# Kernel optimization log

Hardware: AMD Instinct MI355X
Metric: run time of the kernel (lower is better)

## Reference

```python
import jax, jax.numpy as jnp
import numpy as np

WS = (2, 7, 7)      # window size
SS = (1, 3, 3)      # shift size
NH = 8              # num heads
DIM = 256
N = WS[0] * WS[1] * WS[2]   # 98 tokens per window
EPS = 1e-5


def _ln(x, w, b):
    m = jnp.mean(x, -1, keepdims=True)
    v = jnp.mean((x - m) ** 2, -1, keepdims=True)
    return (x - m) / jnp.sqrt(v + EPS) * w + b


def _rel_index():
    coords = np.stack(np.meshgrid(np.arange(WS[0]), np.arange(WS[1]), np.arange(WS[2]), indexing='ij'))
    cf = coords.reshape(3, -1)
    rc = (cf[:, :, None] - cf[:, None, :]).transpose(1, 2, 0).astype(np.int64)
    rc[..., 0] += WS[0] - 1
    rc[..., 1] += WS[1] - 1
    rc[..., 2] += WS[2] - 1
    rc[..., 0] *= (2 * WS[1] - 1) * (2 * WS[2] - 1)
    rc[..., 1] *= 2 * WS[2] - 1
    return rc.sum(-1).astype(np.int32)  # [N, N]


def _attn_mask(Dp, Hp, Wp):
    img = np.zeros((1, Dp, Hp, Wp, 1), np.float32)
    cnt = 0
    def sl(ws, ss):
        return (slice(0, -ws), slice(-ws, -ss), slice(-ss, None))
    for d in sl(WS[0], SS[0]):
        for h in sl(WS[1], SS[1]):
            for w in sl(WS[2], SS[2]):
                img[:, d, h, w, :] = cnt
                cnt += 1
    mw = img.reshape(1, Dp // WS[0], WS[0], Hp // WS[1], WS[1], Wp // WS[2], WS[2], 1)
    mw = mw.transpose(0, 1, 3, 5, 2, 4, 6, 7).reshape(-1, N)
    am = mw[:, None, :] - mw[:, :, None]
    return np.where(am != 0, np.float32(-100.0), np.float32(0.0)).astype(np.float32)  # [nW, N, N]


def setup_inputs() -> dict:
    key = jax.random.key(0)
    ks = jax.random.split(key, 6)
    B, D, H, W, C = 2, 16, 56, 56, DIM
    hid = 4 * C
    return {
        'x': jax.random.normal(ks[0], (B, D, H, W, C), jnp.float32),
        'mask_matrix': jnp.asarray(_attn_mask(D, H, W)),
        'rel_index': jnp.asarray(_rel_index()),
        'rel_bias_table': 0.02 * jax.random.normal(ks[1], ((2 * WS[0] - 1) * (2 * WS[1] - 1) * (2 * WS[2] - 1), NH), jnp.float32),
        'norm1_w': jnp.ones((C,), jnp.float32), 'norm1_b': jnp.zeros((C,), jnp.float32),
        'qkv_w': 0.02 * jax.random.normal(ks[2], (3 * C, C), jnp.float32), 'qkv_b': jnp.zeros((3 * C,), jnp.float32),
        'proj_w': 0.02 * jax.random.normal(ks[3], (C, C), jnp.float32), 'proj_b': jnp.zeros((C,), jnp.float32),
        'norm2_w': jnp.ones((C,), jnp.float32), 'norm2_b': jnp.zeros((C,), jnp.float32),
        'fc1_w': 0.02 * jax.random.normal(ks[4], (hid, C), jnp.float32), 'fc1_b': jnp.zeros((hid,), jnp.float32),
        'fc2_w': 0.02 * jax.random.normal(ks[5], (C, hid), jnp.float32), 'fc2_b': jnp.zeros((C,), jnp.float32),
    }


def _forward(x, mask_matrix, rel_index, rel_bias_table, norm1_w, norm1_b, qkv_w, qkv_b,
             proj_w, proj_b, norm2_w, norm2_b, fc1_w, fc1_b, fc2_w, fc2_b):
    B, D, H, W, C = x.shape
    nh, hd = NH, C // NH
    scale = hd ** -0.5
    nd, nhw, nww = D // WS[0], H // WS[1], W // WS[2]

    # --- part 1: norm -> shift -> window attention -> unshift ---
    h = _ln(x, norm1_w, norm1_b)
    h = jnp.roll(h, (-SS[0], -SS[1], -SS[2]), axis=(1, 2, 3))
    # window partition -> [B_, N, C]
    h = h.reshape(B, nd, WS[0], nhw, WS[1], nww, WS[2], C)
    h = h.transpose(0, 1, 3, 5, 2, 4, 6, 7).reshape(-1, N, C)
    B_ = h.shape[0]

    qkv = (h @ qkv_w.T + qkv_b).reshape(B_, N, 3, nh, hd).transpose(2, 0, 3, 1, 4)
    q, k, v = qkv[0], qkv[1], qkv[2]   # [B_, nh, N, hd]
    attn = jnp.einsum('bhnd,bhmd->bhnm', q * scale, k)
    bias = rel_bias_table[rel_index.reshape(-1)].reshape(N, N, nh).transpose(2, 0, 1)
    attn = attn + bias[None]
    nW = mask_matrix.shape[0]
    attn = attn.reshape(B_ // nW, nW, nh, N, N) + mask_matrix[None, :, None]
    attn = jax.nn.softmax(attn.reshape(B_, nh, N, N), axis=-1)
    o = jnp.einsum('bhnm,bhmd->bhnd', attn, v).transpose(0, 2, 1, 3).reshape(B_, N, C)
    o = o @ proj_w.T + proj_b
    # window reverse -> [B, D, H, W, C]
    o = o.reshape(B, nd, nhw, nww, WS[0], WS[1], WS[2], C)
    o = o.transpose(0, 1, 4, 2, 5, 3, 6, 7).reshape(B, D, H, W, C)
    o = jnp.roll(o, SS, axis=(1, 2, 3))

    x = x + o
    # --- part 2: MLP ---
    h2 = _ln(x, norm2_w, norm2_b)
    h2 = jax.nn.gelu(h2 @ fc1_w.T + fc1_b, approximate=False)
    return x + (h2 @ fc2_w.T + fc2_b)


def reference(x, mask_matrix, rel_index, rel_bias_table, norm1_w, norm1_b, qkv_w, qkv_b,
              proj_w, proj_b, norm2_w, norm2_b, fc1_w, fc1_b, fc2_w, fc2_b):
    return _forward(x, mask_matrix, rel_index, rel_bias_table, norm1_w, norm1_b, qkv_w, qkv_b,
                    proj_w, proj_b, norm2_w, norm2_b, fc1_w, fc1_b, fc2_w, fc2_b)
```

## Files before the change

### kernel.cpp

```cpp
#include <hip/hip_runtime.h>
#include <hip/hip_bf16.h>

typedef __attribute__((ext_vector_type(8))) short bf16x8;
typedef __attribute__((ext_vector_type(4))) float f32x4;

__device__ __forceinline__ unsigned short f2bf(float f){
  __hip_bfloat16 h = __float2bfloat16(f);
  return *reinterpret_cast<unsigned short*>(&h);
}

#define GLDS16(gptr, lptr) \
  __builtin_amdgcn_global_load_lds((const __attribute__((address_space(1))) unsigned int*)(gptr), \
                                   (__attribute__((address_space(3))) unsigned int*)(lptr), 16, 0, 0)

__global__ void cvtk(const float* __restrict__ s, unsigned short* __restrict__ d, int n){
  int i = blockIdx.x*256 + threadIdx.x;
  if (i < n) d[i] = f2bf(s[i]);
}

__global__ void cvt2k(const float* __restrict__ s1, int n1, const float* __restrict__ s2, int n2,
                      unsigned short* __restrict__ d){
  int i = blockIdx.x*256 + threadIdx.x;
  if (i < n1) d[i] = f2bf(s1[i]);
  else if (i < n1 + n2) d[i] = f2bf(s2[i - n1]);
}

__global__ void combok(const int* __restrict__ ri, const float* __restrict__ tbl,
                       const float* __restrict__ mask, unsigned short* __restrict__ out){
  int g = blockIdx.x*256 + threadIdx.x;
  if (g >= 802816) return;
  int r = g & 3;
  int t = g >> 2;
  int lane = t & 63; t >>= 6;
  int nt = t % 7; t /= 7;
  int mt = t % 7; t /= 7;
  int p = t >> 3, h = t & 7;
  int gi = mt*16 + (lane >> 4)*4 + r; if (gi > 97) gi = 97;
  int j  = nt*16 + (lane & 15);
  float v;
  if (j < 98){
    int wrep = ((p&4)?448:0) + ((p&2)?56:0) + ((p&1)?7:0);
    v = tbl[ri[gi*98 + j]*8 + h] + mask[(size_t)wrep*9604 + gi*98 + j];
  } else {
    v = -30000.f;
  }
  out[g] = f2bf(v);
}

__launch_bounds__(256)
__global__ void lnk(const float* __restrict__ xin, const float* __restrict__ gw, const float* __restrict__ gb,
                    unsigned short* __restrict__ hout, int mode)
{
  int wid = threadIdx.x >> 6, lane = threadIdx.x & 63;
  int tok = blockIdx.x*4 + wid;
  int src;
  if (mode == 0){
    int w = tok / 98, n = tok % 98;
    int b = w >> 9, rr = w & 511;
    int di = rr >> 6, hi = (rr >> 3) & 7, wi = rr & 7;
    int d2 = n / 49, n2 = n % 49, h2 = n2 / 7, w2 = n2 % 7;
    int sd = (di*2 + d2 + 1) & 15;
    int sh = hi*7 + h2 + 3; if (sh >= 56) sh -= 56;
    int sw = wi*7 + w2 + 3; if (sw >= 56) sw -= 56;
    src = ((b*16 + sd)*56 + sh)*56 + sw;
  } else {
    src = tok;
  }
  float4 v = *(const float4*)(xin + (size_t)src*256 + lane*4);
  float s  = v.x + v.y + v.z + v.w;
  float s2 = v.x*v.x + v.y*v.y + v.z*v.z + v.w*v.w;
  #pragma unroll
  for (int off = 1; off < 64; off <<= 1){
    s  += __shfl_xor(s, off);
    s2 += __shfl_xor(s2, off);
  }
  float mean = s * (1.f/256.f);
  float var  = s2 * (1.f/256.f) - mean*mean;
  float rstd = rsqrtf(var + 1e-5f);
  int c = lane*4;
  float4 wv = *(const float4*)(gw + c);
  float4 bv = *(const float4*)(gb + c);
  unsigned int p0 = (unsigned int)f2bf((v.x-mean)*rstd*wv.x + bv.x)
                  | ((unsigned int)f2bf((v.y-mean)*rstd*wv.y + bv.y) << 16);
  unsigned int p1 = (unsigned int)f2bf((v.z-mean)*rstd*wv.z + bv.z)
                  | ((unsigned int)f2bf((v.w-mean)*rstd*wv.w + bv.w) << 16);
  uint2 pk; pk.x = p0; pk.y = p1;
  *(uint2*)(hout + (size_t)tok*256 + c) = pk;
}

template<int EPI>
__launch_bounds__(256, 4)
__global__ void gemmk(const unsigned short* __restrict__ A, const unsigned short* __restrict__ Bw,
                      const float* __restrict__ bias, int K, int nbx,
                      unsigned short* __restrict__ outb, const float* __restrict__ xres,
                      float* __restrict__ outf, int moff)
{
  __shared__ unsigned short As[2][4096];
  __shared__ unsigned short Bs[2][4096];
  int tid = threadIdx.x;
  int wid = tid >> 6, lane = tid & 63, l16 = lane & 15, lk = lane >> 4;
  int wm = wid >> 1, wn = wid & 1;
  int cpx = gridDim.x >> 3;
  int swb = (blockIdx.x & 7)*cpx + (blockIdx.x >> 3);
  int mblk = swb / nbx, nblk = swb % nbx;
  const unsigned short* Ab = A  + (size_t)mblk*128*K;
  const unsigned short* Bb = Bw + (size_t)nblk*128*K;
  int rA = tid >> 2;
  int rB = ((rA & 15) << 2) + ((rA >> 4) & 3);
  int kcA = (((tid & 3) ^ ((tid >> 3) & 3)))*8;
  int sx = (l16 >> 1) & 3;

#define STAGE(bufi, kss) do { \
    GLDS16(Ab + (size_t)rA*K      + (kss) + kcA, &As[bufi][wid*512]); \
    GLDS16(Ab + (size_t)(rA+64)*K + (kss) + kcA, &As[bufi][2048 + wid*512]); \
    GLDS16(Bb + (size_t)rB*K      + (kss) + kcA, &Bs[bufi][wid*512]); \
    GLDS16(Bb + (size_t)(rB+64)*K + (kss) + kcA, &Bs[bufi][2048 + wid*512]); \
  } while(0)

  f32x4 acc[4][4];
  #pragma unroll
  for (int i = 0; i < 4; i++)
    #pragma unroll
    for (int j = 0; j < 4; j++)
      acc[i][j] = (f32x4){0.f,0.f,0.f,0.f};

  STAGE(0, 0);
  int cur = 0;
  for (int ks = 0; ks < K; ks += 32){
    if (ks + 32 < K){
      STAGE(cur ^ 1, ks + 32);
      asm volatile("s_waitcnt vmcnt(4)" ::: "memory");
    } else {
      asm volatile("s_waitcnt vmcnt(0)" ::: "memory");
    }
    __builtin_amdgcn_s_barrier();
    __builtin_amdgcn_sched_barrier(0);
    bf16x8 af[4], bfr[4];
    #pragma unroll
    for (int mi = 0; mi < 4; mi++) af[mi]  = *(const bf16x8*)&As[cur][(wm*64 + mi*16 + l16)*32 + (lk ^ sx)*8];
    #pragma unroll
    for (int ni = 0; ni < 4; ni++) bfr[ni] = *(const bf16x8*)&Bs[cur][(wn*64 + ni*16 + l16)*32 + (lk ^ sx)*8];
    #pragma unroll
    for (int mi = 0; mi < 4; mi++)
      #pragma unroll
      for (int ni = 0; ni < 4; ni++)
        acc[mi][ni] = __builtin_amdgcn_mfma_f32_16x16x32_bf16(af[mi], bfr[ni], acc[mi][ni], 0, 0, 0);
    __builtin_amdgcn_sched_barrier(0);
    __builtin_amdgcn_s_barrier();
    cur ^= 1;
  }
#undef STAGE

  int rowb = mblk*128 + wm*64;
  int colb = nblk*128 + wn*64;
  int c4 = colb + 4*l16;
  float4 bv = *(const float4*)(bias + c4);
  #pragma unroll
  for (int mi = 0; mi < 4; mi++){
    #pragma unroll
    for (int r = 0; r < 4; r++){
      int row = rowb + mi*16 + lk*4 + r;
      float v0 = acc[mi][0][r] + bv.x;
      float v1 = acc[mi][1][r] + bv.y;
      float v2 = acc[mi][2][r] + bv.z;
      float v3 = acc[mi][3][r] + bv.w;
      if constexpr (EPI == 0){
        if (colb < 256){
          const float sc = 0.17677669529663687f;
          v0 *= sc; v1 *= sc; v2 *= sc; v3 *= sc;
        }
        uint2 pk;
        pk.x = (unsigned int)f2bf(v0) | ((unsigned int)f2bf(v1) << 16);
        pk.y = (unsigned int)f2bf(v2) | ((unsigned int)f2bf(v3) << 16);
        *(uint2*)(outb + (size_t)row*768 + c4) = pk;
      } else if constexpr (EPI == 1){
        int w = row / 98, n = row % 98;
        int b = w >> 9, rr = w & 511;
        int di = rr >> 6, hi = (rr >> 3) & 7, wi = rr & 7;
        int d2 = n / 49, n2 = n % 49, h2 = n2 / 7, w2 = n2 % 7;
        int sd = (di*2 + d2 + 1) & 15;
        int sh = hi*7 + h2 + 3; if (sh >= 56) sh -= 56;
        int sw = wi*7 + w2 + 3; if (sw >= 56) sw -= 56;
        size_t tnat = (((size_t)b*16 + sd)*56 + sh)*56 + sw;
        float4 xr = *(const float4*)(xres + tnat*256 + c4);
        float4 ov;
        ov.x = xr.x + v0; ov.y = xr.y + v1; ov.z = xr.z + v2; ov.w = xr.w + v3;
        *(float4*)(outf + tnat*256 + c4) = ov;
      } else if constexpr (EPI == 2){
        float g0 = v0 * 0.5f * (1.f + erff(v0 * 0.70710678118654752f));
        float g1 = v1 * 0.5f * (1.f + erff(v1 * 0.70710678118654752f));
        float g2 = v2 * 0.5f * (1.f + erff(v2 * 0.70710678118654752f));
        float g3 = v3 * 0.5f * (1.f + erff(v3 * 0.70710678118654752f));
        uint2 pk;
        pk.x = (unsigned int)f2bf(g0) | ((unsigned int)f2bf(g1) << 16);
        pk.y = (unsigned int)f2bf(g2) | ((unsigned int)f2bf(g3) << 16);
        *(uint2*)(outb + (size_t)row*1024 + c4) = pk;
      } else {
        float* p = outf + (size_t)(moff + row)*256 + c4;
        float4 cu = *(const float4*)p;
        cu.x += v0; cu.y += v1; cu.z += v2; cu.w += v3;
        *(float4*)p = cu;
      }
    }
  }
}

__launch_bounds__(256)
__global__ void attnk(const unsigned short* __restrict__ qkv, const unsigned short* __restrict__ comboX,
                      unsigned short* __restrict__ obuf)
{
  __shared__ unsigned short P[4][16*136];
  int tid = threadIdx.x, wid = tid >> 6, lane = tid & 63, l16 = lane & 15, lk = lane >> 4;
  int cpx = gridDim.x >> 3;
  int swb = (blockIdx.x & 7)*cpx + (blockIdx.x >> 3);
  int task = swb*4 + wid;
  int w = task >> 3, h = task & 7;
  int rr = w & 511;
  int pat = (((rr>>6)==7)?4:0) | ((((rr>>3)&7)==7)?2:0) | (((rr&7)==7)?1:0);
  const unsigned short* cb = comboX + (size_t)(pat*8 + h)*12544;
  const unsigned short* base = qkv + (size_t)w*98*768 + h*32;

  bf16x8 kfr[7];
  #pragma unroll
  for (int nt = 0; nt < 7; nt++){
    int kc = nt*16 + l16; if (kc > 97) kc = 97;
    kfr[nt] = *(const bf16x8*)(base + (size_t)kc*768 + 256 + lk*8);
  }
  bf16x8 v0[4], v1[4];
  #pragma unroll
  for (int kcc = 0; kcc < 4; kcc++){
    #pragma unroll
    for (int j = 0; j < 8; j++){
      int k = kcc*32 + lk*8 + j; if (k > 97) k = 97;
      unsigned int u = *(const unsigned int*)(base + (size_t)k*768 + 512 + 2*l16);
      v0[kcc][j] = (short)(u & 0xffff);
      v1[kcc][j] = (short)(u >> 16);
    }
  }
  bf16x8 vones;
  #pragma unroll
  for (int j = 0; j < 8; j++) vones[j] = (short)0x3F80;

  unsigned short* Pw = &P[wid][0];
  { int rp = lane >> 2, cc = 112 + (lane & 3)*4;
    *(uint2*)&Pw[rp*136 + cc] = make_uint2(0u, 0u); }

  for (int mt = 0; mt < 7; mt++){
    int qrow = mt*16 + l16; if (qrow > 97) qrow = 97;
    bf16x8 qa = *(const bf16x8*)(base + (size_t)qrow*768 + lk*8);

    const unsigned short* cm = cb + mt*1792;
    f32x4 s[7];
    #pragma unroll
    for (int nt = 0; nt < 7; nt++){
      uint2 c2 = *(const uint2*)(cm + (nt*64 + lane)*4);
      f32x4 ci;
      ci[0] = __uint_as_float(c2.x << 16);
      ci[1] = __uint_as_float(c2.x & 0xffff0000u);
      ci[2] = __uint_as_float(c2.y << 16);
      ci[3] = __uint_as_float(c2.y & 0xffff0000u);
      s[nt] = __builtin_amdgcn_mfma_f32_16x16x32_bf16(qa, kfr[nt], ci, 0, 0, 0);
    }

    float mx[4] = {-3e38f,-3e38f,-3e38f,-3e38f};
    #pragma unroll
    for (int nt = 0; nt < 7; nt++){
      mx[0] = fmaxf(mx[0], s[nt][0]); mx[1] = fmaxf(mx[1], s[nt][1]);
      mx[2] = fmaxf(mx[2], s[nt][2]); mx[3] = fmaxf(mx[3], s[nt][3]);
    }
    float mxa = fmaxf(fmaxf(mx[0], mx[1]), fmaxf(mx[2], mx[3]));
    #pragma unroll
    for (int off = 1; off < 64; off <<= 1) mxa = fmaxf(mxa, __shfl_xor(mxa, off));

    #pragma unroll
    for (int r = 0; r < 4; r++)
      #pragma unroll
      for (int nt = 0; nt < 7; nt++)
        Pw[(lk*4 + r)*136 + nt*16 + l16] = f2bf(__expf(s[nt][r] - mxa));

    f32x4 o0 = (f32x4){0.f,0.f,0.f,0.f}, o1 = (f32x4){0.f,0.f,0.f,0.f};
    f32x4 os = (f32x4){0.f,0.f,0.f,0.f};
    #pragma unroll
    for (int kcc = 0; kcc < 4; kcc++){
      bf16x8 pa = *(const bf16x8*)&Pw[l16*136 + kcc*32 + lk*8];
      __builtin_amdgcn_s_setprio(1);
      o0 = __builtin_amdgcn_mfma_f32_16x16x32_bf16(pa, v0[kcc], o0, 0, 0, 0);
      o1 = __builtin_amdgcn_mfma_f32_16x16x32_bf16(pa, v1[kcc], o1, 0, 0, 0);
      os = __builtin_amdgcn_mfma_f32_16x16x32_bf16(pa, vones,   os, 0, 0, 0);
      __builtin_amdgcn_s_setprio(0);
    }
    #pragma unroll
    for (int r = 0; r < 4; r++){
      int n = mt*16 + lk*4 + r;
      if (n < 98){
        float inv = __builtin_amdgcn_rcpf(os[r]);
        unsigned int pk = (unsigned int)f2bf(o0[r]*inv) | ((unsigned int)f2bf(o1[r]*inv) << 16);
        *(unsigned int*)(obuf + ((size_t)w*98 + n)*256 + h*32 + 2*l16) = pk;
      }
    }
  }
}

extern "C" void kernel_launch(void* const* d_in, const int* in_sizes, int n_in,
                              void* d_out, int out_size, void* d_ws, size_t ws_size,
                              hipStream_t stream)
{
  const float* x     = (const float*)d_in[0];
  const float* maskm = (const float*)d_in[1];
  const int*   ri    = (const int*)d_in[2];
  const float* tbl   = (const float*)d_in[3];
  const float* n1w   = (const float*)d_in[4];
  const float* n1b   = (const float*)d_in[5];
  const float* qkvw  = (const float*)d_in[6];
  const float* qkvbv = (const float*)d_in[7];
  const float* projw = (const float*)d_in[8];
  const float* projb = (const float*)d_in[9];
  const float* n2w   = (const float*)d_in[10];
  const float* n2b   = (const float*)d_in[11];
  const float* fc1w  = (const float*)d_in[12];
  const float* fc1b  = (const float*)d_in[13];
  const float* fc2w  = (const float*)d_in[14];
  const float* fc2b  = (const float*)d_in[15];
  float* dout = (float*)d_out;
  char* ws = (char*)d_ws;

  unsigned short* qkvB  = (unsigned short*)(ws + 0);
  unsigned short* hb    = (unsigned short*)(ws + 154140672);
  unsigned short* wq    = (unsigned short*)(ws + 205520896);
  unsigned short* comboX= (unsigned short*)(ws + 205914112);
  unsigned short* wp    = (unsigned short*)(ws + 0);
  unsigned short* h2 = (unsigned short*)(ws + 0);
  unsigned short* g  = (unsigned short*)(ws + 51380224);
  unsigned short* w1 = (unsigned short*)(ws + 154140672);
  unsigned short* w2 = (unsigned short*)(ws + 154664960);

  cvtk<<<768, 256, 0, stream>>>(qkvw, wq, 196608);
  combok<<<3136, 256, 0, stream>>>(ri, tbl, maskm, comboX);

  lnk<<<25088, 256, 0, stream>>>(x, n1w, n1b, hb, 0);
  gemmk<0><<<784*6, 256, 0, stream>>>(hb, wq, qkvbv, 256, 6, qkvB, nullptr, nullptr, 0);
  attnk<<<2048, 256, 0, stream>>>(qkvB, comboX, hb);
  cvtk<<<256, 256, 0, stream>>>(projw, wp, 65536);
  gemmk<1><<<784*2, 256, 0, stream>>>(hb, wp, projb, 256, 2, nullptr, x, dout, 0);

  cvt2k<<<2048, 256, 0, stream>>>(fc1w, 262144, fc2w, 262144, w1);
  lnk<<<25088, 256, 0, stream>>>(dout, n2w, n2b, h2, 1);
  for (int c = 0; c < 2; c++){
    gemmk<2><<<392*8, 256, 0, stream>>>(h2 + (size_t)c*50176*256, w1, fc1b, 256, 8, g, nullptr, nullptr, 0);
    gemmk<3><<<392*2, 256, 0, stream>>>(g, w2, fc2b, 1024, 2, nullptr, nullptr, dout, c*50176);
  }
}
```

Before: 465.8 us.

## Fuse proj GEMM residual add with LayerNorm2 into one full-width kernel

Result: slower. 483.8 us (+3.9%).

```diff
diff --git a/kernel.cpp b/kernel.cpp
--- a/kernel.cpp
+++ b/kernel.cpp
@@ -49,23 +49,19 @@
 
 __launch_bounds__(256)
 __global__ void lnk(const float* __restrict__ xin, const float* __restrict__ gw, const float* __restrict__ gb,
-                    unsigned short* __restrict__ hout, int mode)
+                    unsigned short* __restrict__ hout)
 {
   int wid = threadIdx.x >> 6, lane = threadIdx.x & 63;
   int tok = blockIdx.x*4 + wid;
-  int src;
-  if (mode == 0){
-    int w = tok / 98, n = tok % 98;
-    int b = w >> 9, rr = w & 511;
-    int di = rr >> 6, hi = (rr >> 3) & 7, wi = rr & 7;
-    int d2 = n / 49, n2 = n % 49, h2 = n2 / 7, w2 = n2 % 7;
-    int sd = (di*2 + d2 + 1) & 15;
-    int sh = hi*7 + h2 + 3; if (sh >= 56) sh -= 56;
-    int sw = wi*7 + w2 + 3; if (sw >= 56) sw -= 56;
-    src = ((b*16 + sd)*56 + sh)*56 + sw;
-  } else {
-    src = tok;
-  }
+  int w = tok / 98, n = tok % 98;
+  int b = w >> 9, rr = w & 511;
+  int di = rr >> 6, hi = (rr >> 3) & 7, wi = rr & 7;
+  int d2 = n / 49, n2 = n % 49, h2 = n2 / 7, w2 = n2 % 7;
+  int sd = (di*2 + d2 + 1) & 15;
+  int sh = hi*7 + h2 + 3; if (sh >= 56) sh -= 56;
+  int sw = wi*7 + w2 + 3; if (sw >= 56) sw -= 56;
+  int src = ((b*16 + sd)*56 + sh)*56 + sw;
+
   float4 v = *(const float4*)(xin + (size_t)src*256 + lane*4);
   float s  = v.x + v.y + v.z + v.w;
   float s2 = v.x*v.x + v.y*v.y + v.z*v.z + v.w*v.w;
@@ -92,8 +88,7 @@
 __launch_bounds__(256, 4)
 __global__ void gemmk(const unsigned short* __restrict__ A, const unsigned short* __restrict__ Bw,
                       const float* __restrict__ bias, int K, int nbx,
-                      unsigned short* __restrict__ outb, const float* __restrict__ xres,
-                      float* __restrict__ outf, int moff)
+                      unsigned short* __restrict__ outb, float* __restrict__ outf, int moff)
 {
   __shared__ unsigned short As[2][4096];
   __shared__ unsigned short Bs[2][4096];
@@ -173,19 +168,6 @@
         pk.x = (unsigned int)f2bf(v0) | ((unsigned int)f2bf(v1) << 16);
         pk.y = (unsigned int)f2bf(v2) | ((unsigned int)f2bf(v3) << 16);
         *(uint2*)(outb + (size_t)row*768 + c4) = pk;
-      } else if constexpr (EPI == 1){
-        int w = row / 98, n = row % 98;
-        int b = w >> 9, rr = w & 511;
-        int di = rr >> 6, hi = (rr >> 3) & 7, wi = rr & 7;
-        int d2 = n / 49, n2 = n % 49, h2 = n2 / 7, w2 = n2 % 7;
-        int sd = (di*2 + d2 + 1) & 15;
-        int sh = hi*7 + h2 + 3; if (sh >= 56) sh -= 56;
-        int sw = wi*7 + w2 + 3; if (sw >= 56) sw -= 56;
-        size_t tnat = (((size_t)b*16 + sd)*56 + sh)*56 + sw;
-        float4 xr = *(const float4*)(xres + tnat*256 + c4);
-        float4 ov;
-        ov.x = xr.x + v0; ov.y = xr.y + v1; ov.z = xr.z + v2; ov.w = xr.w + v3;
-        *(float4*)(outf + tnat*256 + c4) = ov;
       } else if constexpr (EPI == 2){
         float g0 = v0 * 0.5f * (1.f + erff(v0 * 0.70710678118654752f));
         float g1 = v1 * 0.5f * (1.f + erff(v1 * 0.70710678118654752f));
@@ -201,6 +183,162 @@
         cu.x += v0; cu.y += v1; cu.z += v2; cu.w += v3;
         *(float4*)p = cu;
       }
+    }
+  }
+}
+
+__launch_bounds__(256, 2)
+__global__ void gemmk1f(const unsigned short* __restrict__ A, const unsigned short* __restrict__ Bw,
+                        const float* __restrict__ bias, const float* __restrict__ xres,
+                        float* __restrict__ dout, unsigned short* __restrict__ h2out,
+                        const float* __restrict__ n2w, const float* __restrict__ n2b)
+{
+  __shared__ unsigned short As[2][4096];
+  __shared__ unsigned short Bs[2][8192];
+  __shared__ float stat[2][2][64][2];
+  const int K = 256;
+  int tid = threadIdx.x;
+  int wid = tid >> 6, lane = tid & 63, l16 = lane & 15, lk = lane >> 4;
+  int wm = wid >> 1, wn = wid & 1;
+  int cpx = gridDim.x >> 3;
+  int mblk = (blockIdx.x & 7)*cpx + (blockIdx.x >> 3);
+  const unsigned short* Ab = A + (size_t)mblk*128*K;
+  int rA = tid >> 2;
+  int rB = ((rA & 15) << 2) + ((rA >> 4) & 3);
+  int kcA = (((tid & 3) ^ ((tid >> 3) & 3)))*8;
+  int sx = (l16 >> 1) & 3;
+
+#define STG1F(bufi, kss) do { \
+    GLDS16(Ab + (size_t)rA*K        + (kss) + kcA, &As[bufi][wid*512]); \
+    GLDS16(Ab + (size_t)(rA+64)*K   + (kss) + kcA, &As[bufi][2048 + wid*512]); \
+    GLDS16(Bw + (size_t)rB*K        + (kss) + kcA, &Bs[bufi][wid*512]); \
+    GLDS16(Bw + (size_t)(rB+64)*K   + (kss) + kcA, &Bs[bufi][2048 + wid*512]); \
+    GLDS16(Bw + (size_t)(rB+128)*K  + (kss) + kcA, &Bs[bufi][4096 + wid*512]); \
+    GLDS16(Bw + (size_t)(rB+192)*K  + (kss) + kcA, &Bs[bufi][6144 + wid*512]); \
+  } while(0)
+
+  f32x4 acc[4][8];
+  #pragma unroll
+  for (int i = 0; i < 4; i++)
+    #pragma unroll
+    for (int j = 0; j < 8; j++)
+      acc[i][j] = (f32x4){0.f,0.f,0.f,0.f};
+
+  STG1F(0, 0);
+  int cur = 0;
+  for (int ks = 0; ks < K; ks += 32){
+    if (ks + 32 < K){
+      STG1F(cur ^ 1, ks + 32);
+      asm volatile("s_waitcnt vmcnt(6)" ::: "memory");
+    } else {
+      asm volatile("s_waitcnt vmcnt(0)" ::: "memory");
+    }
+    __builtin_amdgcn_s_barrier();
+    __builtin_amdgcn_sched_barrier(0);
+    bf16x8 af[4], bfr[8];
+    #pragma unroll
+    for (int mi = 0; mi < 4; mi++) af[mi]  = *(const bf16x8*)&As[cur][(wm*64 + mi*16 + l16)*32 + (lk ^ sx)*8];
+    #pragma unroll
+    for (int n8 = 0; n8 < 8; n8++) bfr[n8] = *(const bf16x8*)&Bs[cur][(wn*128 + n8*16 + l16)*32 + (lk ^ sx)*8];
+    #pragma unroll
+    for (int mi = 0; mi < 4; mi++)
+      #pragma unroll
+      for (int n8 = 0; n8 < 8; n8++)
+        acc[mi][n8] = __builtin_amdgcn_mfma_f32_16x16x32_bf16(af[mi], bfr[n8], acc[mi][n8], 0, 0, 0);
+    __builtin_amdgcn_sched_barrier(0);
+    __builtin_amdgcn_s_barrier();
+    cur ^= 1;
+  }
+#undef STG1F
+
+  int rowb = mblk*128 + wm*64;
+  int c4 = wn*128 + 4*l16;
+  float4 bva = *(const float4*)(bias + c4);
+  float4 bvb = *(const float4*)(bias + c4 + 64);
+
+  float rs[4][4], rs2[4][4];
+  int   tn[4][4];
+  #pragma unroll
+  for (int mi = 0; mi < 4; mi++){
+    #pragma unroll
+    for (int r = 0; r < 4; r++){
+      int row = rowb + mi*16 + lk*4 + r;
+      int w = row / 98, n = row % 98;
+      int b = w >> 9, rr = w & 511;
+      int di = rr >> 6, hi = (rr >> 3) & 7, wi = rr & 7;
+      int d2 = n / 49, n2 = n % 49, hh = n2 / 7, w2 = n2 % 7;
+      int sd = (di*2 + d2 + 1) & 15;
+      int sh = hi*7 + hh + 3; if (sh >= 56) sh -= 56;
+      int sw = wi*7 + w2 + 3; if (sw >= 56) sw -= 56;
+      int tnat = ((b*16 + sd)*56 + sh)*56 + sw;
+      tn[mi][r] = tnat;
+      float4 xr0 = *(const float4*)(xres + (size_t)tnat*256 + c4);
+      float4 xr1 = *(const float4*)(xres + (size_t)tnat*256 + c4 + 64);
+      float4 va, vb2;
+      va.x  = acc[mi][0][r] + bva.x + xr0.x;
+      va.y  = acc[mi][1][r] + bva.y + xr0.y;
+      va.z  = acc[mi][2][r] + bva.z + xr0.z;
+      va.w  = acc[mi][3][r] + bva.w + xr0.w;
+      vb2.x = acc[mi][4][r] + bvb.x + xr1.x;
+      vb2.y = acc[mi][5][r] + bvb.y + xr1.y;
+      vb2.z = acc[mi][6][r] + bvb.z + xr1.z;
+      vb2.w = acc[mi][7][r] + bvb.w + xr1.w;
+      *(float4*)(dout + (size_t)tnat*256 + c4)      = va;
+      *(float4*)(dout + (size_t)tnat*256 + c4 + 64) = vb2;
+      float s  = va.x + va.y + va.z + va.w + vb2.x + vb2.y + vb2.z + vb2.w;
+      float s2 = va.x*va.x + va.y*va.y + va.z*va.z + va.w*va.w
+               + vb2.x*vb2.x + vb2.y*vb2.y + vb2.z*vb2.z + vb2.w*vb2.w;
+      rs[mi][r] = s; rs2[mi][r] = s2;
+    }
+  }
+  #pragma unroll
+  for (int mi = 0; mi < 4; mi++)
+    #pragma unroll
+    for (int r = 0; r < 4; r++){
+      #pragma unroll
+      for (int off = 1; off < 16; off <<= 1){
+        rs[mi][r]  += __shfl_xor(rs[mi][r],  off);
+        rs2[mi][r] += __shfl_xor(rs2[mi][r], off);
+      }
+    }
+  if (l16 == 0){
+    #pragma unroll
+    for (int mi = 0; mi < 4; mi++)
+      #pragma unroll
+      for (int r = 0; r < 4; r++){
+        stat[wm][wn][mi*16 + lk*4 + r][0] = rs[mi][r];
+        stat[wm][wn][mi*16 + lk*4 + r][1] = rs2[mi][r];
+      }
+  }
+  __syncthreads();
+  float4 w2a = *(const float4*)(n2w + c4);
+  float4 w2b = *(const float4*)(n2w + c4 + 64);
+  float4 b2a = *(const float4*)(n2b + c4);
+  float4 b2b = *(const float4*)(n2b + c4 + 64);
+  #pragma unroll
+  for (int mi = 0; mi < 4; mi++){
+    #pragma unroll
+    for (int r = 0; r < 4; r++){
+      int r64 = mi*16 + lk*4 + r;
+      float so  = rs[mi][r]  + stat[wm][wn^1][r64][0];
+      float so2 = rs2[mi][r] + stat[wm][wn^1][r64][1];
+      float mean = so * (1.f/256.f);
+      float var  = so2 * (1.f/256.f) - mean*mean;
+      float rstd = rsqrtf(var + 1e-5f);
+      int tnat = tn[mi][r];
+      float4 va  = *(const float4*)(dout + (size_t)tnat*256 + c4);
+      float4 vb2 = *(const float4*)(dout + (size_t)tnat*256 + c4 + 64);
+      uint2 pk0, pk1;
+      pk0.x = (unsigned int)f2bf((va.x-mean)*rstd*w2a.x + b2a.x)
+            | ((unsigned int)f2bf((va.y-mean)*rstd*w2a.y + b2a.y) << 16);
+      pk0.y = (unsigned int)f2bf((va.z-mean)*rstd*w2a.z + b2a.z)
+            | ((unsigned int)f2bf((va.w-mean)*rstd*w2a.w + b2a.w) << 16);
+      pk1.x = (unsigned int)f2bf((vb2.x-mean)*rstd*w2b.x + b2b.x)
+            | ((unsigned int)f2bf((vb2.y-mean)*rstd*w2b.y + b2b.y) << 16);
+      pk1.y = (unsigned int)f2bf((vb2.z-mean)*rstd*w2b.z + b2b.z)
+            | ((unsigned int)f2bf((vb2.w-mean)*rstd*w2b.w + b2b.w) << 16);
+      *(uint2*)(h2out + (size_t)tnat*256 + c4)      = pk0;
+      *(uint2*)(h2out + (size_t)tnat*256 + c4 + 64) = pk1;
     }
   }
 }
@@ -328,25 +466,24 @@
   unsigned short* hb    = (unsigned short*)(ws + 154140672);
   unsigned short* wq    = (unsigned short*)(ws + 205520896);
   unsigned short* comboX= (unsigned short*)(ws + 205914112);
-  unsigned short* wp    = (unsigned short*)(ws + 0);
-  unsigned short* h2 = (unsigned short*)(ws + 0);
-  unsigned short* g  = (unsigned short*)(ws + 51380224);
-  unsigned short* w1 = (unsigned short*)(ws + 154140672);
-  unsigned short* w2 = (unsigned short*)(ws + 154664960);
+  unsigned short* wp = (unsigned short*)(ws + 0);
+  unsigned short* w1 = (unsigned short*)(ws + 131072);
+  unsigned short* w2 = (unsigned short*)(ws + 655360);
+  unsigned short* h2 = (unsigned short*)(ws + 2097152);
+  unsigned short* g  = (unsigned short*)(ws + 53477376);
 
   cvtk<<<768, 256, 0, stream>>>(qkvw, wq, 196608);
   combok<<<3136, 256, 0, stream>>>(ri, tbl, maskm, comboX);
 
-  lnk<<<25088, 256, 0, stream>>>(x, n1w, n1b, hb, 0);
-  gemmk<0><<<784*6, 256, 0, stream>>>(hb, wq, qkvbv, 256, 6, qkvB, nullptr, nullptr, 0);
+  lnk<<<25088, 256, 0, stream>>>(x, n1w, n1b, hb);
+  gemmk<0><<<784*6, 256, 0, stream>>>(hb, wq, qkvbv, 256, 6, qkvB, nullptr, 0);
   attnk<<<2048, 256, 0, stream>>>(qkvB, comboX, hb);
   cvtk<<<256, 256, 0, stream>>>(projw, wp, 65536);
-  gemmk<1><<<784*2, 256, 0, stream>>>(hb, wp, projb, 256, 2, nullptr, x, dout, 0);
-
   cvt2k<<<2048, 256, 0, stream>>>(fc1w, 262144, fc2w, 262144, w1);
-  lnk<<<25088, 256, 0, stream>>>(dout, n2w, n2b, h2, 1);
+  gemmk1f<<<784, 256, 0, stream>>>(hb, wp, projb, x, dout, h2, n2w, n2b);
+
   for (int c = 0; c < 2; c++){
-    gemmk<2><<<392*8, 256, 0, stream>>>(h2 + (size_t)c*50176*256, w1, fc1b, 256, 8, g, nullptr, nullptr, 0);
-    gemmk<3><<<392*2, 256, 0, stream>>>(g, w2, fc2b, 1024, 2, nullptr, nullptr, dout, c*50176);
-  }
-}
+    gemmk<2><<<392*8, 256, 0, stream>>>(h2 + (size_t)c*50176*256, w1, fc1b, 256, 8, g, nullptr, 0);
+    gemmk<3><<<392*2, 256, 0, stream>>>(g, w2, fc2b, 1024, 2, nullptr, dout, c*50176);
+  }
+}
```
